# Kernel optimization log

Measured on AMD Instinct MI355X. Metric: run time of the kernel, lower is better.

## Reference

```python
import math
import jax, jax.numpy as jnp
from jax import lax
import numpy as np

B, N, D, H, L, F = 128, 200, 128, 8, 3, 2048


def setup_inputs():
    key = jax.random.key(0)
    ks = jax.random.split(key, 24)
    g = lambda i, shape: (0.05 * jax.random.normal(ks[i], shape)).astype(jnp.float32)
    coords = jax.random.uniform(ks[0], (B, N, 2), dtype=jnp.float32)
    demands = jax.random.uniform(ks[1], (B, N), minval=1.0, maxval=10.0, dtype=jnp.float32)
    demands = demands.at[:, 0].set(0.0)  # depot demand = 0
    capacity = jnp.full((B,), 50.0, jnp.float32)
    return dict(
        coords=coords, demands_raw=demands, capacity_raw=capacity,
        embed_W=g(2, (D, 3)), embed_b=g(3, (D,)),
        Wqkv=g(4, (L, 3 * D, D)), bqkv=g(5, (L, 3 * D)),
        Wo=g(6, (L, D, D)), bo=g(7, (L, D)),
        W1=g(8, (L, F, D)), b1=g(9, (L, F)),
        W2=g(10, (L, D, F)), b2=g(11, (L, D)),
        ln1_g=jnp.ones((L, D), jnp.float32), ln1_b=jnp.zeros((L, D), jnp.float32),
        ln2_g=jnp.ones((L, D), jnp.float32), ln2_b=jnp.zeros((L, D), jnp.float32),
        Wq=g(12, (D, D)), Wk=g(13, (D, D)),
        Wcap=g(14, (D, 1)), bcap=g(15, (D,)),
        Wctx=g(16, (D, 3 * D)), bctx=g(17, (D,)),
    )


def _ln(x, g, b):
    m = x.mean(-1, keepdims=True)
    v = ((x - m) ** 2).mean(-1, keepdims=True)
    return (x - m) / jnp.sqrt(v + 1e-5) * g + b


def _forward(coords, demands_raw, capacity_raw, embed_W, embed_b, Wqkv, bqkv, Wo, bo,
             W1, b1, W2, b2, ln1_g, ln1_b, ln2_g, ln2_b, Wq, Wk, Wcap, bcap, Wctx, bctx):
    Bd, Nd, _ = coords.shape
    cap = capacity_raw.reshape(Bd, 1)
    demand_ratio = demands_raw / cap                       # (B,N)
    x = jnp.concatenate([coords, demand_ratio[..., None]], -1)  # (B,N,3)
    h = x @ embed_W.T + embed_b                            # (B,N,D)
    d = h.shape[-1]
    dh = d // H
    # --- transformer encoder (post-LN, relu FFN), eval mode (no dropout) ---
    for i in range(Wqkv.shape[0]):
        qkv = h @ Wqkv[i].T + bqkv[i]
        q, k, v = jnp.split(qkv, 3, -1)
        q = q.reshape(Bd, Nd, H, dh)
        k = k.reshape(Bd, Nd, H, dh)
        v = v.reshape(Bd, Nd, H, dh)
        s = jnp.einsum('bqhd,bkhd->bhqk', q, k) / math.sqrt(dh)
        a = jax.nn.softmax(s, -1)
        o = jnp.einsum('bhqk,bkhd->bqhd', a, v).reshape(Bd, Nd, d) @ Wo[i].T + bo[i]
        h = _ln(h + o, ln1_g[i], ln1_b[i])
        f = jax.nn.relu(h @ W1[i].T + b1[i]) @ W2[i].T + b2[i]
        h = _ln(h + f, ln2_g[i], ln2_b[i])
    global_ctx = h.mean(1)                                 # (B,D)
    kmat = h @ Wk.T                                        # K cache: static across steps
    sqrt_d = math.sqrt(d)
    max_steps = 2 * (Nd - 1) + 1
    ar = jnp.arange(Bd)

    def step(carry, _):
        current, visited, remaining, done, key = carry
        key, sk = jax.random.split(key)
        cur_h = h[ar, current]                             # (B,D)
        cap_h = remaining @ Wcap.T + bcap                  # (B,D)
        q_in = jnp.concatenate([cur_h, global_ctx, cap_h], -1)
        q = (q_in @ Wctx.T + bctx) @ Wq.T                  # (B,D)
        logits = (kmat * q[:, None, :]).sum(-1) / sqrt_d   # (B,N)
        infeasible = visited | (demand_ratio > remaining)
        feas_cust = (~visited[:, 1:]) & (demand_ratio[:, 1:] <= remaining)
        has_feas = feas_cust.any(1)
        all_served = visited[:, 1:].all(1)
        force_depot = all_served & (current != 0) & (~done)
        at_depot = (current == 0) & (~done)
        not_depot = (current != 0) & (~done)
        # prevent_early_return=True path
        depot_mask = (at_depot & has_feas) | (not_depot & has_feas & (~all_served))
        infeasible = infeasible.at[:, 0].set(infeasible[:, 0] | depot_mask)
        force_depot = force_depot | (not_depot & (~has_feas)) | done
        masked = jnp.where(infeasible, -1e9, logits)
        logp = jax.nn.log_softmax(masked, -1)
        sel = jax.random.categorical(sk, masked)           # sampling decode
        sel_logp = logp[ar, sel]
        sel = jnp.where(force_depot, 0, sel)
        sel_logp = jnp.where(force_depot, 0.0, sel_logp)
        is_depot = sel == 0
        take = demand_ratio[ar, sel][:, None]
        remaining = jnp.clip(jnp.where(is_depot[:, None], 1.0, remaining - take), 0.0, 1.0)
        visited = visited.at[ar, sel].set(visited[ar, sel] | (~is_depot))
        done = done | (visited[:, 1:].all(1) & (sel == 0))
        return (sel, visited, remaining, done, key), (sel, sel_logp)

    init = (jnp.zeros(Bd, jnp.int32), jnp.zeros((Bd, Nd), bool),
            jnp.ones((Bd, 1), coords.dtype), jnp.zeros(Bd, bool), jax.random.key(42))
    _, (acts, lps) = lax.scan(step, init, None, length=max_steps)
    path = jnp.concatenate([jnp.zeros((Bd, 1), jnp.int32), acts.T], 1)  # (B, 1+max_steps)
    logps = lps.sum(0)                                                  # (B,)
    return path, logps


def reference(coords, demands_raw, capacity_raw, embed_W, embed_b, Wqkv, bqkv, Wo, bo,
              W1, b1, W2, b2, ln1_g, ln1_b, ln2_g, ln2_b, Wq, Wk, Wcap, bcap, Wctx, bctx):
    return _forward(coords, demands_raw, capacity_raw, embed_W, embed_b, Wqkv, bqkv, Wo, bo,
                    W1, b1, W2, b2, ln1_g, ln1_b, ln2_g, ln2_b, Wq, Wk, Wcap, bcap, Wctx, bctx)
```

## Files before the change

### kernel.cpp

```cpp
#include <hip/hip_runtime.h>
#include <hip/hip_bf16.h>
#include <stdint.h>
#include <math.h>

#define NB 128
#define NN 200
#define ND 128
#define NH 8
#define DH 16
#define NL 3
#define NF 2048
#define NT (NB * NN)
#define NSTEP 399

__host__ __device__ inline void tf2x32(unsigned k0, unsigned k1, unsigned x0, unsigned x1,
                                       unsigned* o0, unsigned* o1) {
  unsigned ks[3] = {k0, k1, k0 ^ k1 ^ 0x1BD11BDAu};
  x0 += ks[0]; x1 += ks[1];
  const unsigned R[2][4] = {{13u, 15u, 26u, 6u}, {17u, 29u, 16u, 24u}};
#pragma unroll
  for (int i = 0; i < 5; ++i) {
#pragma unroll
    for (int j = 0; j < 4; ++j) {
      unsigned r = R[i & 1][j];
      x0 += x1;
      x1 = (x1 << r) | (x1 >> (32u - r));
      x1 ^= x0;
    }
    x0 += ks[(i + 1) % 3];
    x1 += ks[(i + 2) % 3] + (unsigned)(i + 1);
  }
  *o0 = x0; *o1 = x1;
}

__global__ void k_rng(unsigned* __restrict__ rng) {
  unsigned k0 = 0u, k1 = 42u;
  for (int t = 0; t < NSTEP; ++t) {
    unsigned a0, a1, s0, s1;
    tf2x32(k0, k1, 0u, 1u, &s0, &s1);
    tf2x32(k0, k1, 0u, 0u, &a0, &a1);
    rng[2 * t] = s0; rng[2 * t + 1] = s1;
    k0 = a0; k1 = a1;
  }
}

__global__ __launch_bounds__(256) void k_gum(const unsigned* __restrict__ rng, float* __restrict__ gum) {
  int idx = blockIdx.x * 256 + threadIdx.x;
  if (idx >= NSTEP * NT) return;
  int t = idx / NT, j = idx - t * NT;
  unsigned o0, o1;
  tf2x32(rng[2 * t], rng[2 * t + 1], 0u, (unsigned)j, &o0, &o1);
  unsigned bits = o0 ^ o1;
  float u01 = __uint_as_float((bits >> 9) | 0x3f800000u) - 1.0f;
  float uu = fmaxf(1.17549435082228751e-38f, u01);
  gum[idx] = (float)(-log(-log((double)uu)));
}

__global__ void k_tr(const float* __restrict__ src, float* __restrict__ dst, int R, int C) {
  int i = blockIdx.x * 256 + threadIdx.x;
  if (i >= R * C) return;
  int c = i / R, r = i - c * R;
  dst[i] = src[(size_t)r * C + c];
}

__global__ void k_embed(const float* __restrict__ coords, const float* __restrict__ dem,
                        const float* __restrict__ cap, const float* __restrict__ eW,
                        const float* __restrict__ eb, float* __restrict__ h, float* __restrict__ dr) {
  int gid = blockIdx.x * blockDim.x + threadIdx.x;
  int t = gid >> 7, d = gid & 127;
  int b = t / NN;
  float drv = dem[t] / cap[b];
  double acc = (double)eW[d * 3] * (double)coords[2 * t]
             + (double)eW[d * 3 + 1] * (double)coords[2 * t + 1]
             + (double)eW[d * 3 + 2] * (double)drv;
  h[gid] = (float)acc + eb[d];
  if (d == 0) dr[t] = drv;
}

#define QT 8
__global__ __launch_bounds__(384) void k_qkv(const float* __restrict__ h, const float* __restrict__ WT,
                                             const float* __restrict__ bias, float* __restrict__ qkv) {
  const int t0 = blockIdx.x * QT, j = threadIdx.x;
  __shared__ double hsh[ND][QT];
  for (int idx = j; idx < ND * QT; idx += 384) {
    int t = idx & 7, k = idx >> 3;
    hsh[k][t] = (double)h[(size_t)(t0 + t) * ND + k];
  }
  __syncthreads();
  double acc[QT];
#pragma unroll
  for (int t = 0; t < QT; ++t) acc[t] = 0.0;
  for (int k = 0; k < ND; ++k) {
    double w = (double)WT[(size_t)k * 384 + j];
#pragma unroll
    for (int t = 0; t < QT; ++t) acc[t] += w * hsh[k][t];
  }
  float bv = bias[j];
#pragma unroll
  for (int t = 0; t < QT; ++t)
    qkv[(size_t)(t0 + t) * 384 + j] = (float)acc[t] + bv;
}

__global__ __launch_bounds__(256) void k_attn(const float* __restrict__ qkv, float* __restrict__ att) {
  const int b = blockIdx.x / NH, hh = blockIdx.x % NH, tid = threadIdx.x;
  const int lane = tid & 63, w = tid >> 6;
  __shared__ float qsh[NN][DH + 1];
  __shared__ float ksh[NN][DH + 1];
  __shared__ float vsh[NN][DH + 1];
  __shared__ float ashw[4][NN + 8];
  for (int idx = tid; idx < NN * DH; idx += 256) {
    int n = idx / DH, d2 = idx % DH;
    size_t base = (size_t)(b * NN + n) * 384 + hh * DH + d2;
    qsh[n][d2] = qkv[base];
    ksh[n][d2] = qkv[base + ND];
    vsh[n][d2] = qkv[base + 2 * ND];
  }
  __syncthreads();
  const int dd = lane & 15, q4 = lane >> 4;
  for (int qn = w; qn < NN; qn += 4) {
    double qv[DH];
#pragma unroll
    for (int d = 0; d < DH; ++d) qv[d] = (double)qsh[qn][d];
    float sf[4];
#pragma unroll
    for (int s = 0; s < 4; ++s) {
      int n = lane + 64 * s;
      if (n < NN) {
        double a = 0.0;
#pragma unroll
        for (int d = 0; d < DH; ++d) a += qv[d] * (double)ksh[n][d];
        sf[s] = (float)a / 4.0f;
      } else sf[s] = -3.0e38f;
    }
    float m = fmaxf(fmaxf(sf[0], sf[1]), fmaxf(sf[2], sf[3]));
    for (int off = 1; off < 64; off <<= 1) m = fmaxf(m, __shfl_xor(m, off, 64));
    double e[4];
    double esum = 0.0;
#pragma unroll
    for (int s = 0; s < 4; ++s) {
      int n = lane + 64 * s;
      e[s] = (n < NN) ? exp((double)(sf[s] - m)) : 0.0;
      esum += e[s];
    }
    for (int off = 1; off < 64; off <<= 1) esum += __shfl_xor(esum, off, 64);
#pragma unroll
    for (int s = 0; s < 4; ++s) {
      int n = lane + 64 * s;
      if (n < NN) ashw[w][n] = (float)(e[s] / esum);
    }
    double o = 0.0;
    for (int i = 0; i < 50; ++i) {
      int n = q4 * 50 + i;
      o += (double)ashw[w][n] * (double)vsh[n][dd];
    }
    o += __shfl_xor(o, 16, 64);
    o += __shfl_xor(o, 32, 64);
    if (lane < DH)
      att[(size_t)(b * NN + qn) * ND + hh * DH + lane] = (float)o;
  }
}

#define OT 4
__global__ __launch_bounds__(128) void k_oln(const float* __restrict__ att, const float* __restrict__ WoT,
                                             const float* __restrict__ bo, const float* __restrict__ g,
                                             const float* __restrict__ bb, float* __restrict__ h) {
  const int t0 = blockIdx.x * OT, d = threadIdx.x;
  __shared__ double ash[ND][OT];
  __shared__ float xsh[OT][ND];
  __shared__ float mred[OT], sred[OT];
  for (int idx = d; idx < ND * OT; idx += 128) {
    int t = idx & 3, k = idx >> 2;
    ash[k][t] = (double)att[(size_t)(t0 + t) * ND + k];
  }
  __syncthreads();
  double acc[OT];
#pragma unroll
  for (int t = 0; t < OT; ++t) acc[t] = 0.0;
  for (int k = 0; k < ND; ++k) {
    double w = (double)WoT[(size_t)k * ND + d];
#pragma unroll
    for (int t = 0; t < OT; ++t) acc[t] += w * ash[k][t];
  }
  float bv = bo[d];
#pragma unroll
  for (int t = 0; t < OT; ++t) {
    float o = (float)acc[t] + bv;
    xsh[t][d] = h[(size_t)(t0 + t) * ND + d] + o;
  }
  __syncthreads();
  if (d < OT) {
    double sv = 0.0;
    for (int k = 0; k < ND; ++k) sv += (double)xsh[d][k];
    float m = (float)(sv / 128.0);
    double sq = 0.0;
    for (int k = 0; k < ND; ++k) { float tf = xsh[d][k] - m; sq += (double)tf * (double)tf; }
    mred[d] = m;
    sred[d] = sqrtf((float)(sq / 128.0) + 1e-5f);
  }
  __syncthreads();
#pragma unroll
  for (int t = 0; t < OT; ++t) {
    float tf = xsh[t][d] - mred[t];
    h[(size_t)(t0 + t) * ND + d] = tf / sred[t] * g[d] + bb[d];
  }
}

#define FT 8
#define JC 1024
__global__ __launch_bounds__(256) void k_ffn(float* __restrict__ h, const float* __restrict__ W1T,
                                             const float* __restrict__ b1, const float* __restrict__ W2T,
                                             const float* __restrict__ b2, const float* __restrict__ g,
                                             const float* __restrict__ bb) {
  const int t0 = blockIdx.x * FT, tid = threadIdx.x;
  __shared__ double hsh[ND][FT];
  __shared__ double fsh[FT][JC];
  __shared__ float xsh[FT][ND];
  __shared__ float mred[FT], sred[FT];
  for (int idx = tid; idx < ND * FT; idx += 256) {
    int t = idx & 7, k = idx >> 3;
    hsh[k][t] = (double)h[(size_t)(t0 + t) * ND + k];
  }
  __syncthreads();
  const int jg = tid >> 5, dl = tid & 31;
  double acc2[4][FT];
#pragma unroll
  for (int a = 0; a < 4; ++a)
#pragma unroll
    for (int t = 0; t < FT; ++t) acc2[a][t] = 0.0;
  for (int c = 0; c < 2; ++c) {
    {
      const int j0 = tid * 4;
      double acc[4][FT];
#pragma unroll
      for (int a = 0; a < 4; ++a)
#pragma unroll
        for (int t = 0; t < FT; ++t) acc[a][t] = 0.0;
      for (int k = 0; k < ND; ++k) {
        double hv[FT];
#pragma unroll
        for (int t = 0; t < FT; ++t) hv[t] = hsh[k][t];
        float4 wa = *(const float4*)(W1T + (size_t)k * NF + c * JC + j0);
        double wd[4] = {(double)wa.x, (double)wa.y, (double)wa.z, (double)wa.w};
#pragma unroll
        for (int a = 0; a < 4; ++a)
#pragma unroll
          for (int t = 0; t < FT; ++t) acc[a][t] += wd[a] * hv[t];
      }
#pragma unroll
      for (int a = 0; a < 4; ++a) {
        float bv = b1[c * JC + j0 + a];
#pragma unroll
        for (int t = 0; t < FT; ++t) {
          float f = (float)acc[a][t] + bv;
          fsh[t][j0 + a] = (double)fmaxf(f, 0.0f);
        }
      }
    }
    __syncthreads();
    for (int i = 0; i < 128; ++i) {
      int jj = (jg << 7) | ((i + jg) & 127);
      int j = c * JC + jj;
      double fv[FT];
#pragma unroll
      for (int t = 0; t < FT; ++t) fv[t] = fsh[t][jj];
      float4 wv = *(const float4*)(W2T + (size_t)j * ND + (dl << 2));
      double wd[4] = {(double)wv.x, (double)wv.y, (double)wv.z, (double)wv.w};
#pragma unroll
      for (int a = 0; a < 4; ++a)
#pragma unroll
        for (int t = 0; t < FT; ++t) acc2[a][t] += wd[a] * fv[t];
    }
    __syncthreads();
  }
  double* red = &fsh[0][0];
#pragma unroll
  for (int a = 0; a < 4; ++a)
#pragma unroll
    for (int t = 0; t < FT; ++t)
      red[(((jg * 8 + t) << 7)) + (dl << 2) + a] = acc2[a][t];
  __syncthreads();
  for (int idx = tid; idx < ND * FT; idx += 256) {
    int t = idx >> 7, d = idx & 127;
    double s = 0.0;
#pragma unroll
    for (int jg2 = 0; jg2 < 8; ++jg2) s += red[((jg2 * 8 + t) << 7) + d];
    float o = (float)s + b2[d];
    float hf = (float)hsh[d][t];
    xsh[t][d] = hf + o;
  }
  __syncthreads();
  if (tid < FT) {
    double sv = 0.0;
    for (int d = 0; d < ND; ++d) sv += (double)xsh[tid][d];
    float m = (float)(sv / 128.0);
    double sq = 0.0;
    for (int d = 0; d < ND; ++d) { float tf = xsh[tid][d] - m; sq += (double)tf * (double)tf; }
    mred[tid] = m;
    sred[tid] = sqrtf((float)(sq / 128.0) + 1e-5f);
  }
  __syncthreads();
  for (int idx = tid; idx < ND * FT; idx += 256) {
    int d = idx & 127, t = idx >> 7;
    float tf = xsh[t][d] - mred[t];
    h[(size_t)(t0 + t) * ND + d] = tf / sred[t] * g[d] + bb[d];
  }
}

__global__ __launch_bounds__(128) void k_gctx(const float* __restrict__ h, float* __restrict__ gctx) {
  int b = blockIdx.x, d = threadIdx.x;
  double acc = 0.0;
  for (int n = 0; n < NN; ++n) acc += (double)h[(size_t)(b * NN + n) * ND + d];
  gctx[b * ND + d] = (float)(acc / 200.0);
}

#define KT 8
__global__ __launch_bounds__(128) void k_kmat(const float* __restrict__ h, const float* __restrict__ WkT,
                                              float* __restrict__ kmat) {
  const int t0 = blockIdx.x * KT, d = threadIdx.x;
  __shared__ double hsh[ND][KT];
  for (int idx = d; idx < ND * KT; idx += 128) {
    int t = idx & 7, k = idx >> 3;
    hsh[k][t] = (double)h[(size_t)(t0 + t) * ND + k];
  }
  __syncthreads();
  double acc[KT];
#pragma unroll
  for (int t = 0; t < KT; ++t) acc[t] = 0.0;
  for (int k = 0; k < ND; ++k) {
    double w = (double)WkT[(size_t)k * ND + d];
#pragma unroll
    for (int t = 0; t < KT; ++t) acc[t] += w * hsh[k][t];
  }
#pragma unroll
  for (int t = 0; t < KT; ++t)
    kmat[(size_t)(t0 + t) * ND + d] = (float)acc[t];
}

__global__ __launch_bounds__(128) void k_prep1(const float* __restrict__ Wctx, const float* __restrict__ bcap,
                                               const float* __restrict__ Wcap, const float* __restrict__ bctx,
                                               double* __restrict__ t1, double* __restrict__ wu) {
  int k = threadIdx.x;
  double a = 0.0, c = 0.0;
  for (int m = 0; m < ND; ++m) {
    double wc = (double)Wctx[(size_t)k * 384 + 256 + m];
    a += wc * (double)bcap[m];
    c += wc * (double)Wcap[m];
  }
  t1[k] = a + (double)bctx[k];
  wu[k] = c;
}

__global__ __launch_bounds__(128) void k_M(const float* __restrict__ Wq, const float* __restrict__ Wctx,
                                           double* __restrict__ M) {
  int d = blockIdx.x, j = threadIdx.x;
  double acc = 0.0;
  for (int k = 0; k < ND; ++k)
    acc += (double)Wq[(size_t)d * ND + k] * (double)Wctx[(size_t)k * 384 + j];
  M[(size_t)d * ND + j] = acc;
}

__global__ __launch_bounds__(128) void k_u(const float* __restrict__ Wq, const double* __restrict__ wu,
                                           double* __restrict__ u) {
  int d = threadIdx.x;
  double acc = 0.0;
  for (int k = 0; k < ND; ++k) acc += (double)Wq[(size_t)d * ND + k] * wu[k];
  u[d] = acc;
}

__global__ __launch_bounds__(128) void k_t2(const float* __restrict__ Wctx, const float* __restrict__ gctx,
                                            double* __restrict__ t2) {
  int b = blockIdx.x, k = threadIdx.x;
  double acc = 0.0;
  for (int m = 0; m < ND; ++m)
    acc += (double)Wctx[(size_t)k * 384 + 128 + m] * (double)gctx[b * ND + m];
  t2[(size_t)b * ND + k] = acc;
}

__global__ __launch_bounds__(128) void k_vb(const float* __restrict__ Wq, const double* __restrict__ t2,
                                            const double* __restrict__ t1, double* __restrict__ vb) {
  int b = blockIdx.x, d = threadIdx.x;
  double acc = 0.0;
  for (int k = 0; k < ND; ++k)
    acc += (double)Wq[(size_t)d * ND + k] * (t2[(size_t)b * ND + k] + t1[k]);
  vb[(size_t)b * ND + d] = acc;
}

__global__ __launch_bounds__(256) void k_c01(const float* __restrict__ kmat, const double* __restrict__ vb,
                                             const double* __restrict__ u, float* __restrict__ c0, float* __restrict__ c1) {
  int t = blockIdx.x * 256 + threadIdx.x;
  if (t >= NT) return;
  int b = t / NN;
  double a0 = 0.0, a1 = 0.0;
  for (int d = 0; d < ND; ++d) {
    double km = (double)kmat[(size_t)t * ND + d];
    a0 += km * vb[(size_t)b * ND + d];
    a1 += km * u[d];
  }
  c0[t] = (float)a0;
  c1[t] = (float)a1;
}

__global__ __launch_bounds__(128) void k_KM(const float* __restrict__ kmat, const double* __restrict__ M,
                                            float* __restrict__ KM) {
  const int t0 = blockIdx.x * KT, j = threadIdx.x;
  __shared__ double ksh[ND][KT];
  for (int idx = j; idx < ND * KT; idx += 128) {
    int t = idx & 7, k = idx >> 3;
    ksh[k][t] = (double)kmat[(size_t)(t0 + t) * ND + k];
  }
  __syncthreads();
  double acc[KT];
#pragma unroll
  for (int t = 0; t < KT; ++t) acc[t] = 0.0;
  for (int d = 0; d < ND; ++d) {
    double m = M[(size_t)d * ND + j];
#pragma unroll
    for (int t = 0; t < KT; ++t) acc[t] += ksh[d][t] * m;
  }
#pragma unroll
  for (int t = 0; t < KT; ++t)
    KM[(size_t)(t0 + t) * ND + j] = (float)acc[t];
}

__global__ __launch_bounds__(256) void k_P(const float* __restrict__ KM, const float* __restrict__ h,
                                           float* __restrict__ P) {
  int blk = blockIdx.x, tid = threadIdx.x;
  int b = blk / NN;
  __shared__ float hrow[ND];
  if (tid < ND) hrow[tid] = h[(size_t)blk * ND + tid];
  __syncthreads();
  if (tid < NN) {
    const float* kr = KM + (size_t)(b * NN + tid) * ND;
    double acc = 0.0;
    for (int j = 0; j < ND; ++j) acc += (double)kr[j] * (double)hrow[j];
    P[(size_t)blk * NN + tid] = (float)acc;
  }
}

__global__ __launch_bounds__(64) void k_decode(const float* __restrict__ P, const float* __restrict__ c0,
                                               const float* __restrict__ c1, const float* __restrict__ dr,
                                               const float* __restrict__ gum, float* __restrict__ out) {
  __shared__ float Psh[NN * NN];
  const int b = blockIdx.x, l = threadIdx.x;
  {
    const float4* src = (const float4*)(P + (size_t)b * NN * NN);
    float4* dst = (float4*)Psh;
    for (int i = l; i < (NN * NN) / 4; i += 64) dst[i] = src[i];
  }
  float drs4[4], c04[4], c14[4];
  int vis4[4];
#pragma unroll
  for (int s = 0; s < 4; ++s) {
    int n = l + 64 * s;
    bool valid = n < NN;
    drs4[s] = valid ? dr[b * NN + n] : 1e9f;
    c04[s] = valid ? c0[b * NN + n] : 0.0f;
    c14[s] = valid ? c1[b * NN + n] : 0.0f;
    vis4[s] = valid ? 0 : 1;
  }
  int cur = 0, done = 0;
  float rem = 1.0f, lpsum = 0.0f;
  if (l == 0) out[(size_t)b * 400] = 0.0f;
  __syncthreads();
  const float SQD = 11.3137084989847603f;
  float gv4[4];
#pragma unroll
  for (int s = 0; s < 4; ++s) {
    int n = l + 64 * s;
    gv4[s] = (n < NN) ? gum[(size_t)0 * NT + b * NN + n] : 0.0f;
  }
  for (int t = 0; t < NSTEP; ++t) {
    float gn4[4];
    if (t + 1 < NSTEP) {
      const float* grow = gum + (size_t)(t + 1) * NT + b * NN;
#pragma unroll
      for (int s = 0; s < 4; ++s) {
        int n = l + 64 * s;
        gn4[s] = (n < NN) ? grow[n] : 0.0f;
      }
    }
    const float* Prow = Psh + cur * NN;
    float Pv4[4];
#pragma unroll
    for (int s = 0; s < 4; ++s) {
      int n = l + 64 * s;
      Pv4[s] = (n < NN) ? Prow[n] : 0.0f;
    }
    bool lf = false, lns = false;
#pragma unroll
    for (int s = 0; s < 4; ++s) {
      int n = l + 64 * s;
      if (n >= 1 && n < NN && !vis4[s]) {
        lns = true;
        if (drs4[s] <= rem) lf = true;
      }
    }
    const int has_feas = (__ballot(lf) != 0ULL);
    const int all_served = (__ballot(lns) == 0ULL);
    const bool at_depot = (cur == 0) && !done, not_depot = (cur != 0) && !done;
    const bool depot_mask = (at_depot && has_feas) || (not_depot && has_feas && !all_served);
    float msk[4], sc[4];
#pragma unroll
    for (int s = 0; s < 4; ++s) {
      int n = l + 64 * s;
      if (n < NN) {
        double sd = (double)Pv4[s] + (double)c04[s] + (double)rem * (double)c14[s];
        float logit = (float)sd / SQD;
        bool infn = vis4[s] || (drs4[s] > rem) || (n == 0 && depot_mask);
        msk[s] = infn ? -1e9f : logit;
        sc[s] = msk[s] + gv4[s];
      } else {
        msk[s] = -3.0e38f;
        sc[s] = -3.0e38f;
      }
    }
    float bs = sc[0]; int bn = l; float bmsk = msk[0]; float mx = msk[0];
#pragma unroll
    for (int s = 1; s < 4; ++s) {
      int n = l + 64 * s;
      if (sc[s] > bs) { bs = sc[s]; bn = n; bmsk = msk[s]; }
      mx = fmaxf(mx, msk[s]);
    }
    for (int off = 1; off < 64; off <<= 1) {
      float os = __shfl_xor(bs, off, 64);
      int on = __shfl_xor(bn, off, 64);
      float ob = __shfl_xor(bmsk, off, 64);
      float om = __shfl_xor(mx, off, 64);
      if (os > bs || (os == bs && on < bn)) { bs = os; bn = on; bmsk = ob; }
      mx = fmaxf(mx, om);
    }
    float e = 0.0f;
#pragma unroll
    for (int s = 0; s < 4; ++s) e += expf(msk[s] - mx);
    for (int off = 1; off < 64; off <<= 1) e += __shfl_xor(e, off, 64);
    int sel = bn;
    float slp = (bmsk - mx) - logf(e);
    bool force = (all_served && cur != 0 && !done) || (not_depot && !has_feas) || done;
    if (force) { sel = 0; slp = 0.0f; }
    if (l == 0) out[(size_t)b * 400 + 1 + t] = (float)sel;
    lpsum += slp;
    bool isd = (sel == 0);
    float cand = drs4[sel >> 6];
    float take = __shfl(cand, sel & 63, 64);
    float nr = isd ? 1.0f : (rem - take);
    rem = fminf(fmaxf(nr, 0.0f), 1.0f);
    if (!isd && (sel & 63) == l) vis4[sel >> 6] = 1;
    if (all_served && sel == 0) done = 1;
    cur = sel;
#pragma unroll
    for (int s = 0; s < 4; ++s) gv4[s] = gn4[s];
  }
  if (l == 0) out[(size_t)NB * 400 + b] = lpsum;
}

extern "C" void kernel_launch(void* const* d_in, const int* in_sizes, int n_in,
                              void* d_out, int out_size, void* d_ws, size_t ws_size,
                              hipStream_t stream) {
  (void)in_sizes; (void)n_in; (void)out_size; (void)ws_size;
  const float* coords = (const float*)d_in[0];
  const float* dem    = (const float*)d_in[1];
  const float* cap    = (const float*)d_in[2];
  const float* eW     = (const float*)d_in[3];
  const float* eb     = (const float*)d_in[4];
  const float* Wqkv   = (const float*)d_in[5];
  const float* bqkv   = (const float*)d_in[6];
  const float* Wo     = (const float*)d_in[7];
  const float* bo     = (const float*)d_in[8];
  const float* W1     = (const float*)d_in[9];
  const float* b1     = (const float*)d_in[10];
  const float* W2     = (const float*)d_in[11];
  const float* b2     = (const float*)d_in[12];
  const float* ln1g   = (const float*)d_in[13];
  const float* ln1b   = (const float*)d_in[14];
  const float* ln2g   = (const float*)d_in[15];
  const float* ln2b   = (const float*)d_in[16];
  const float* Wq     = (const float*)d_in[17];
  const float* Wk     = (const float*)d_in[18];
  const float* Wcap   = (const float*)d_in[19];
  const float* bcap   = (const float*)d_in[20];
  const float* Wctx   = (const float*)d_in[21];
  const float* bctx   = (const float*)d_in[22];

  char* ws = (char*)d_ws;
  size_t off = 0;
  auto take = [&](size_t bytes) -> void* {
    void* p = ws + off;
    off += (bytes + 255) & ~(size_t)255;
    return p;
  };
  float* dr   = (float*)take((size_t)NT * 4);
  float* c0   = (float*)take((size_t)NT * 4);
  float* c1   = (float*)take((size_t)NT * 4);
  float* P    = (float*)take((size_t)NB * NN * NN * 4);
  unsigned* rng = (unsigned*)take((size_t)NSTEP * 2 * 4);
  float* h    = (float*)take((size_t)NT * ND * 4);
  float* qkv  = (float*)take((size_t)NT * 384 * 4);
  float* att  = (float*)take((size_t)NT * ND * 4);
  float* kmat = (float*)take((size_t)NT * ND * 4);
  float* gctx = (float*)take((size_t)NB * ND * 4);
  double* M   = (double*)take((size_t)ND * ND * 8);
  double* u   = (double*)take((size_t)ND * 8);
  double* t1  = (double*)take((size_t)ND * 8);
  double* wu  = (double*)take((size_t)ND * 8);
  double* t2  = (double*)take((size_t)NB * ND * 8);
  double* vb  = (double*)take((size_t)NB * ND * 8);
  float* W1T   = (float*)take((size_t)NL * NF * ND * 4);
  float* W2T   = (float*)take((size_t)NL * NF * ND * 4);
  float* WqkvT = (float*)take((size_t)NL * 384 * ND * 4);
  float* WoT   = (float*)take((size_t)NL * ND * ND * 4);
  float* WkT   = (float*)take((size_t)ND * ND * 4);
  float* KM  = qkv;
  float* gum = h;

  k_rng<<<1, 1, 0, stream>>>(rng);
  for (int i = 0; i < NL; ++i) {
    k_tr<<<(NF * ND + 255) / 256, 256, 0, stream>>>(W1 + (size_t)i * NF * ND, W1T + (size_t)i * NF * ND, NF, ND);
    k_tr<<<(NF * ND + 255) / 256, 256, 0, stream>>>(W2 + (size_t)i * ND * NF, W2T + (size_t)i * ND * NF, ND, NF);
    k_tr<<<(384 * ND + 255) / 256, 256, 0, stream>>>(Wqkv + (size_t)i * 384 * ND, WqkvT + (size_t)i * 384 * ND, 384, ND);
    k_tr<<<(ND * ND + 255) / 256, 256, 0, stream>>>(Wo + (size_t)i * ND * ND, WoT + (size_t)i * ND * ND, ND, ND);
  }
  k_tr<<<(ND * ND + 255) / 256, 256, 0, stream>>>(Wk, WkT, ND, ND);
  k_embed<<<(NT * ND) / 256, 256, 0, stream>>>(coords, dem, cap, eW, eb, h, dr);
  for (int i = 0; i < NL; ++i) {
    k_qkv<<<NT / QT, 384, 0, stream>>>(h, WqkvT + (size_t)i * 384 * ND, bqkv + (size_t)i * 384, qkv);
    k_attn<<<NB * NH, 256, 0, stream>>>(qkv, att);
    k_oln<<<NT / OT, 128, 0, stream>>>(att, WoT + (size_t)i * ND * ND, bo + (size_t)i * ND,
                                       ln1g + (size_t)i * ND, ln1b + (size_t)i * ND, h);
    k_ffn<<<NT / FT, 256, 0, stream>>>(h, W1T + (size_t)i * NF * ND, b1 + (size_t)i * NF,
                                       W2T + (size_t)i * ND * NF, b2 + (size_t)i * ND,
                                       ln2g + (size_t)i * ND, ln2b + (size_t)i * ND);
  }
  k_gctx<<<NB, 128, 0, stream>>>(h, gctx);
  k_kmat<<<NT / KT, 128, 0, stream>>>(h, WkT, kmat);
  k_prep1<<<1, 128, 0, stream>>>(Wctx, bcap, Wcap, bctx, t1, wu);
  k_M<<<ND, 128, 0, stream>>>(Wq, Wctx, M);
  k_u<<<1, 128, 0, stream>>>(Wq, wu, u);
  k_t2<<<NB, 128, 0, stream>>>(Wctx, gctx, t2);
  k_vb<<<NB, 128, 0, stream>>>(Wq, t2, t1, vb);
  k_c01<<<NT / 256, 256, 0, stream>>>(kmat, vb, u, c0, c1);
  k_KM<<<NT / KT, 128, 0, stream>>>(kmat, M, KM);
  k_P<<<NT, 256, 0, stream>>>(KM, h, P);
  k_gum<<<(NSTEP * NT + 255) / 256, 256, 0, stream>>>(rng, gum);
  k_decode<<<NB, 64, 0, stream>>>(P, c0, c1, dr, gum, (float*)d_out);
}
```

Baseline: 5.006 ms.

## Pre-convert weights to double and tile P computation over query rows

Weight transposes now write double-precision copies, so the GEMM kernels load doubles directly instead of converting float weights to double in their inner loops. The cost is twice the weight memory traffic. Separately, KM is stored transposed per batch, and k_P now computes 8 query rows per block from a shared double tile of h. Each KM column load is reused eight times and reads are coalesced across threads, replacing one block per row with a serial per-thread strided dot product.

Result: slower. 5.305 ms (+6.0%).

```diff
diff --git a/kernel.cpp b/kernel.cpp
--- a/kernel.cpp
+++ b/kernel.cpp
@@ -61,6 +61,13 @@
   if (i >= R * C) return;
   int c = i / R, r = i - c * R;
   dst[i] = src[(size_t)r * C + c];
+}
+
+__global__ void k_trd(const float* __restrict__ src, double* __restrict__ dst, int R, int C) {
+  int i = blockIdx.x * 256 + threadIdx.x;
+  if (i >= R * C) return;
+  int c = i / R, r = i - c * R;
+  dst[i] = (double)src[(size_t)r * C + c];
 }
 
 __global__ void k_embed(const float* __restrict__ coords, const float* __restrict__ dem,
@@ -78,7 +85,7 @@
 }
 
 #define QT 8
-__global__ __launch_bounds__(384) void k_qkv(const float* __restrict__ h, const float* __restrict__ WT,
+__global__ __launch_bounds__(384) void k_qkv(const float* __restrict__ h, const double* __restrict__ WT,
                                              const float* __restrict__ bias, float* __restrict__ qkv) {
   const int t0 = blockIdx.x * QT, j = threadIdx.x;
   __shared__ double hsh[ND][QT];
@@ -91,7 +98,7 @@
 #pragma unroll
   for (int t = 0; t < QT; ++t) acc[t] = 0.0;
   for (int k = 0; k < ND; ++k) {
-    double w = (double)WT[(size_t)k * 384 + j];
+    double w = WT[(size_t)k * 384 + j];
 #pragma unroll
     for (int t = 0; t < QT; ++t) acc[t] += w * hsh[k][t];
   }
@@ -161,7 +168,7 @@
 }
 
 #define OT 4
-__global__ __launch_bounds__(128) void k_oln(const float* __restrict__ att, const float* __restrict__ WoT,
+__global__ __launch_bounds__(128) void k_oln(const float* __restrict__ att, const double* __restrict__ WoT,
                                              const float* __restrict__ bo, const float* __restrict__ g,
                                              const float* __restrict__ bb, float* __restrict__ h) {
   const int t0 = blockIdx.x * OT, d = threadIdx.x;
@@ -177,7 +184,7 @@
 #pragma unroll
   for (int t = 0; t < OT; ++t) acc[t] = 0.0;
   for (int k = 0; k < ND; ++k) {
-    double w = (double)WoT[(size_t)k * ND + d];
+    double w = WoT[(size_t)k * ND + d];
 #pragma unroll
     for (int t = 0; t < OT; ++t) acc[t] += w * ash[k][t];
   }
@@ -207,8 +214,8 @@
 
 #define FT 8
 #define JC 1024
-__global__ __launch_bounds__(256) void k_ffn(float* __restrict__ h, const float* __restrict__ W1T,
-                                             const float* __restrict__ b1, const float* __restrict__ W2T,
+__global__ __launch_bounds__(256) void k_ffn(float* __restrict__ h, const double* __restrict__ W1T,
+                                             const float* __restrict__ b1, const double* __restrict__ W2T,
                                              const float* __restrict__ b2, const float* __restrict__ g,
                                              const float* __restrict__ bb) {
   const int t0 = blockIdx.x * FT, tid = threadIdx.x;
@@ -239,8 +246,10 @@
         double hv[FT];
 #pragma unroll
         for (int t = 0; t < FT; ++t) hv[t] = hsh[k][t];
-        float4 wa = *(const float4*)(W1T + (size_t)k * NF + c * JC + j0);
-        double wd[4] = {(double)wa.x, (double)wa.y, (double)wa.z, (double)wa.w};
+        const double* wp = W1T + (size_t)k * NF + c * JC + j0;
+        double2 wa = *(const double2*)wp;
+        double2 wb = *(const double2*)(wp + 2);
+        double wd[4] = {wa.x, wa.y, wb.x, wb.y};
 #pragma unroll
         for (int a = 0; a < 4; ++a)
 #pragma unroll
@@ -263,8 +272,10 @@
       double fv[FT];
 #pragma unroll
       for (int t = 0; t < FT; ++t) fv[t] = fsh[t][jj];
-      float4 wv = *(const float4*)(W2T + (size_t)j * ND + (dl << 2));
-      double wd[4] = {(double)wv.x, (double)wv.y, (double)wv.z, (double)wv.w};
+      const double* wp = W2T + (size_t)j * ND + (dl << 2);
+      double2 w01 = *(const double2*)wp;
+      double2 w23 = *(const double2*)(wp + 2);
+      double wd[4] = {w01.x, w01.y, w23.x, w23.y};
 #pragma unroll
       for (int a = 0; a < 4; ++a)
 #pragma unroll
@@ -314,7 +325,7 @@
 }
 
 #define KT 8
-__global__ __launch_bounds__(128) void k_kmat(const float* __restrict__ h, const float* __restrict__ WkT,
+__global__ __launch_bounds__(128) void k_kmat(const float* __restrict__ h, const double* __restrict__ WkT,
                                               float* __restrict__ kmat) {
   const int t0 = blockIdx.x * KT, d = threadIdx.x;
   __shared__ double hsh[ND][KT];
@@ -327,7 +338,7 @@
 #pragma unroll
   for (int t = 0; t < KT; ++t) acc[t] = 0.0;
   for (int k = 0; k < ND; ++k) {
-    double w = (double)WkT[(size_t)k * ND + d];
+    double w = WkT[(size_t)k * ND + d];
 #pragma unroll
     for (int t = 0; t < KT; ++t) acc[t] += w * hsh[k][t];
   }
@@ -401,8 +412,9 @@
 }
 
 __global__ __launch_bounds__(128) void k_KM(const float* __restrict__ kmat, const double* __restrict__ M,
-                                            float* __restrict__ KM) {
+                                            float* __restrict__ KMT) {
   const int t0 = blockIdx.x * KT, j = threadIdx.x;
+  const int b = t0 / NN, toff = t0 % NN;
   __shared__ double ksh[ND][KT];
   for (int idx = j; idx < ND * KT; idx += 128) {
     int t = idx & 7, k = idx >> 3;
@@ -419,21 +431,34 @@
   }
 #pragma unroll
   for (int t = 0; t < KT; ++t)
-    KM[(size_t)(t0 + t) * ND + j] = (float)acc[t];
-}
-
-__global__ __launch_bounds__(256) void k_P(const float* __restrict__ KM, const float* __restrict__ h,
+    KMT[(size_t)b * ND * NN + (size_t)j * NN + toff + t] = (float)acc[t];
+}
+
+#define PC 8
+__global__ __launch_bounds__(256) void k_P(const float* __restrict__ KMT, const float* __restrict__ h,
                                            float* __restrict__ P) {
-  int blk = blockIdx.x, tid = threadIdx.x;
-  int b = blk / NN;
-  __shared__ float hrow[ND];
-  if (tid < ND) hrow[tid] = h[(size_t)blk * ND + tid];
+  const int blk = blockIdx.x;
+  const int b = blk / 25, c0 = (blk % 25) * PC;
+  const int tid = threadIdx.x;
+  __shared__ double h8[ND][PC];
+  for (int idx = tid; idx < ND * PC; idx += 256) {
+    int t = idx & 7, j = idx >> 3;
+    h8[j][t] = (double)h[(size_t)(b * NN + c0 + t) * ND + j];
+  }
   __syncthreads();
   if (tid < NN) {
-    const float* kr = KM + (size_t)(b * NN + tid) * ND;
-    double acc = 0.0;
-    for (int j = 0; j < ND; ++j) acc += (double)kr[j] * (double)hrow[j];
-    P[(size_t)blk * NN + tid] = (float)acc;
+    double acc[PC];
+#pragma unroll
+    for (int t = 0; t < PC; ++t) acc[t] = 0.0;
+    const float* kb = KMT + (size_t)b * ND * NN + tid;
+    for (int j = 0; j < ND; ++j) {
+      double km = (double)kb[(size_t)j * NN];
+#pragma unroll
+      for (int t = 0; t < PC; ++t) acc[t] += km * h8[j][t];
+    }
+#pragma unroll
+    for (int t = 0; t < PC; ++t)
+      P[(size_t)(b * NN + c0 + t) * NN + tid] = (float)acc[t];
   }
 }
 
@@ -604,22 +629,22 @@
   double* wu  = (double*)take((size_t)ND * 8);
   double* t2  = (double*)take((size_t)NB * ND * 8);
   double* vb  = (double*)take((size_t)NB * ND * 8);
-  float* W1T   = (float*)take((size_t)NL * NF * ND * 4);
-  float* W2T   = (float*)take((size_t)NL * NF * ND * 4);
-  float* WqkvT = (float*)take((size_t)NL * 384 * ND * 4);
-  float* WoT   = (float*)take((size_t)NL * ND * ND * 4);
-  float* WkT   = (float*)take((size_t)ND * ND * 4);
-  float* KM  = qkv;
+  double* W1T   = (double*)take((size_t)NL * NF * ND * 8);
+  double* W2T   = (double*)take((size_t)NL * NF * ND * 8);
+  double* WqkvT = (double*)take((size_t)NL * 384 * ND * 8);
+  double* WoT   = (double*)take((size_t)NL * ND * ND * 8);
+  double* WkT   = (double*)take((size_t)ND * ND * 8);
+  float* KMT = qkv;
   float* gum = h;
 
   k_rng<<<1, 1, 0, stream>>>(rng);
   for (int i = 0; i < NL; ++i) {
-    k_tr<<<(NF * ND + 255) / 256, 256, 0, stream>>>(W1 + (size_t)i * NF * ND, W1T + (size_t)i * NF * ND, NF, ND);
-    k_tr<<<(NF * ND + 255) / 256, 256, 0, stream>>>(W2 + (size_t)i * ND * NF, W2T + (size_t)i * ND * NF, ND, NF);
-    k_tr<<<(384 * ND + 255) / 256, 256, 0, stream>>>(Wqkv + (size_t)i * 384 * ND, WqkvT + (size_t)i * 384 * ND, 384, ND);
-    k_tr<<<(ND * ND + 255) / 256, 256, 0, stream>>>(Wo + (size_t)i * ND * ND, WoT + (size_t)i * ND * ND, ND, ND);
-  }
-  k_tr<<<(ND * ND + 255) / 256, 256, 0, stream>>>(Wk, WkT, ND, ND);
+    k_trd<<<(NF * ND + 255) / 256, 256, 0, stream>>>(W1 + (size_t)i * NF * ND, W1T + (size_t)i * NF * ND, NF, ND);
+    k_trd<<<(NF * ND + 255) / 256, 256, 0, stream>>>(W2 + (size_t)i * ND * NF, W2T + (size_t)i * ND * NF, ND, NF);
+    k_trd<<<(384 * ND + 255) / 256, 256, 0, stream>>>(Wqkv + (size_t)i * 384 * ND, WqkvT + (size_t)i * 384 * ND, 384, ND);
+    k_trd<<<(ND * ND + 255) / 256, 256, 0, stream>>>(Wo + (size_t)i * ND * ND, WoT + (size_t)i * ND * ND, ND, ND);
+  }
+  k_trd<<<(ND * ND + 255) / 256, 256, 0, stream>>>(Wk, WkT, ND, ND);
   k_embed<<<(NT * ND) / 256, 256, 0, stream>>>(coords, dem, cap, eW, eb, h, dr);
   for (int i = 0; i < NL; ++i) {
     k_qkv<<<NT / QT, 384, 0, stream>>>(h, WqkvT + (size_t)i * 384 * ND, bqkv + (size_t)i * 384, qkv);
@@ -638,8 +663,8 @@
   k_t2<<<NB, 128, 0, stream>>>(Wctx, gctx, t2);
   k_vb<<<NB, 128, 0, stream>>>(Wq, t2, t1, vb);
   k_c01<<<NT / 256, 256, 0, stream>>>(kmat, vb, u, c0, c1);
-  k_KM<<<NT / KT, 128, 0, stream>>>(kmat, M, KM);
-  k_P<<<NT, 256, 0, stream>>>(KM, h, P);
+  k_KM<<<NT / KT, 128, 0, stream>>>(kmat, M, KMT);
+  k_P<<<NB * 25, 256, 0, stream>>>(KMT, h, P);
   k_gum<<<(NSTEP * NT + 255) / 256, 256, 0, stream>>>(rng, gum);
   k_decode<<<NB, 64, 0, stream>>>(P, c0, c1, dr, gum, (float*)d_out);
 }
```
